# Kernel tuning notes

Hardware: AMD Instinct MI355X
Metric: run time of the kernel (lower is better)

Reference implementation:

```python
import jax, jax.numpy as jnp
import numpy as np

B, N, M = 262144, 8, 4  # batch, state dim, measurement dim


def _tril_square(x, n):
    """x: (b, n(n+1)/2) linearized lower-tri elems -> L @ L.T, (b, n, n)."""
    i, j = np.tril_indices(n)
    L = jnp.zeros((x.shape[0], n, n), dtype=x.dtype).at[:, i, j].set(x)
    return jnp.einsum('bik,bjk->bij', L, L)


def setup_inputs() -> dict:
    key = jax.random.key(0)
    ks = jax.random.split(key, 7)
    measurement = jax.random.normal(ks[0], (B, M), dtype=jnp.float32)
    state = jax.random.normal(ks[1], (B, N), dtype=jnp.float32)
    # SPD state covariance: A A^T / n + I
    A = jax.random.normal(ks[2], (B, N, N), dtype=jnp.float32) * 0.3
    state_cov = jnp.einsum('bik,bjk->bij', A, A) / N + jnp.eye(N, dtype=jnp.float32)
    F = jnp.eye(N, dtype=jnp.float32) + 0.1 * jax.random.normal(ks[3], (B, N, N), dtype=jnp.float32)
    H = jax.random.normal(ks[4], (B, M, N), dtype=jnp.float32) * 0.5
    process_noise = jax.random.normal(ks[5], (B, N * (N + 1) // 2), dtype=jnp.float32) * 0.1
    measurement_noise = jax.random.normal(ks[6], (B, M * (M + 1) // 2), dtype=jnp.float32) * 0.3
    return {
        'measurement': measurement, 'state': state, 'state_cov': state_cov,
        'F': F, 'H': H,
        'process_noise': process_noise, 'measurement_noise': measurement_noise,
    }


def reference(measurement, state, state_cov, F, H, process_noise, measurement_noise):
    b, n = state.shape
    m = measurement.shape[1]
    Q = _tril_square(process_noise, n)       # (b, n, n) process noise cov
    R = _tril_square(measurement_noise, m)   # (b, m, m) measurement noise cov

    # Predict
    new_state = jnp.einsum('bij,bj->bi', F, state)
    new_state_cov = jnp.einsum('bij,bjk,blk->bil', F, state_cov, F) + Q

    # Update
    prediction = jnp.einsum('bij,bj->bi', H, new_state)
    res = measurement - prediction
    res_cov = jnp.einsum('bij,bjk,blk->bil', H, new_state_cov, H) + R  # (b, m, m)
    PHt = jnp.einsum('bij,bkj->bik', new_state_cov, H)                 # (b, n, m)
    kgain = jnp.matmul(PHt, jnp.linalg.inv(res_cov))                   # (b, n, m)

    upd_state = new_state + jnp.einsum('bij,bj->bi', kgain, res)
    I = jnp.eye(n, dtype=state.dtype)
    upd_cov = jnp.matmul(I - jnp.matmul(kgain, H), new_state_cov)
    return prediction, upd_state, upd_cov
```

## Files before the change

### kernel.cpp

```cpp
#include <hip/hip_runtime.h>

#define DEVINL __device__ __forceinline__

#define TIX(i, j) ((i) * ((i) + 1) / 2 + (j))
#define SYM(arr, i, j) ((i) >= (j) ? arr[TIX(i, j)] : arr[TIX(j, i)])

DEVINL void inv4(const float* m, float* inv) {
    float s0 = m[0] * m[5] - m[1] * m[4];
    float s1 = m[0] * m[6] - m[2] * m[4];
    float s2 = m[0] * m[7] - m[3] * m[4];
    float s3 = m[1] * m[6] - m[2] * m[5];
    float s4 = m[1] * m[7] - m[3] * m[5];
    float s5 = m[2] * m[7] - m[3] * m[6];
    float c5 = m[10] * m[15] - m[11] * m[14];
    float c4 = m[9] * m[15] - m[11] * m[13];
    float c3 = m[9] * m[14] - m[10] * m[13];
    float c2 = m[8] * m[15] - m[11] * m[12];
    float c1 = m[8] * m[14] - m[10] * m[12];
    float c0 = m[8] * m[13] - m[9] * m[12];
    float det = s0 * c5 - s1 * c4 + s2 * c3 + s3 * c2 - s4 * c1 + s5 * c0;
    float id = 1.0f / det;
    inv[0]  = ( m[5] * c5 - m[6] * c4 + m[7] * c3) * id;
    inv[1]  = (-m[1] * c5 + m[2] * c4 - m[3] * c3) * id;
    inv[2]  = ( m[13] * s5 - m[14] * s4 + m[15] * s3) * id;
    inv[3]  = (-m[9] * s5 + m[10] * s4 - m[11] * s3) * id;
    inv[4]  = (-m[4] * c5 + m[6] * c2 - m[7] * c1) * id;
    inv[5]  = ( m[0] * c5 - m[2] * c2 + m[3] * c1) * id;
    inv[6]  = (-m[12] * s5 + m[14] * s2 - m[15] * s1) * id;
    inv[7]  = ( m[8] * s5 - m[10] * s2 + m[11] * s1) * id;
    inv[8]  = ( m[4] * c4 - m[5] * c2 + m[7] * c0) * id;
    inv[9]  = (-m[0] * c4 + m[1] * c2 - m[3] * c0) * id;
    inv[10] = ( m[12] * s4 - m[13] * s2 + m[15] * s0) * id;
    inv[11] = (-m[8] * s4 + m[9] * s2 - m[11] * s0) * id;
    inv[12] = (-m[4] * c3 + m[5] * c1 - m[6] * c0) * id;
    inv[13] = ( m[0] * c3 - m[1] * c1 + m[2] * c0) * id;
    inv[14] = (-m[12] * s3 + m[13] * s1 - m[14] * s0) * id;
    inv[15] = ( m[8] * s3 - m[9] * s1 + m[10] * s0) * id;
}

__global__ __launch_bounds__(64) void ekf_kernel(
    const float* __restrict__ meas,
    const float* __restrict__ state,
    const float* __restrict__ Pin,
    const float* __restrict__ Fin,
    const float* __restrict__ Hin,
    const float* __restrict__ pnin,
    const float* __restrict__ mnin,
    float* __restrict__ out_pred,
    float* __restrict__ out_state,
    float* __restrict__ out_cov)
{
    const int t  = threadIdx.x;
    const int bb = blockIdx.x * 64;
    const int b  = bb + t;

    __shared__ float4 buf[576];

    {
        const float4* g = reinterpret_cast<const float4*>(pnin) + (size_t)bb * 9;
        #pragma unroll
        for (int i = 0; i < 9; ++i) buf[i * 64 + t] = g[i * 64 + t];
    }
    __syncthreads();
    float Pn[36];
    {
        float Lq[36];
        #pragma unroll
        for (int q = 0; q < 9; ++q) {
            float4 v = buf[t * 9 + q];
            Lq[4 * q] = v.x; Lq[4 * q + 1] = v.y; Lq[4 * q + 2] = v.z; Lq[4 * q + 3] = v.w;
        }
        #pragma unroll
        for (int i = 0; i < 8; ++i)
            #pragma unroll
            for (int j = 0; j <= i; ++j) {
                float acc = 0.f;
                #pragma unroll
                for (int k = 0; k <= j; ++k)
                    acc += Lq[TIX(i, k)] * Lq[TIX(j, k)];
                Pn[TIX(i, j)] = acc;
            }
    }

    {
        const float4* g = reinterpret_cast<const float4*>(state) + (size_t)bb * 2;
        #pragma unroll
        for (int i = 0; i < 2; ++i) {
            int f = i * 64 + t;
            buf[(f >> 1) * 3 + (f & 1)] = g[f];
        }
    }
    __syncthreads();
    float s[8];
    {
        float4 a = buf[t * 3 + 0], c = buf[t * 3 + 1];
        s[0] = a.x; s[1] = a.y; s[2] = a.z; s[3] = a.w;
        s[4] = c.x; s[5] = c.y; s[6] = c.z; s[7] = c.w;
    }

    float Ps[36];
    #pragma unroll
    for (int h = 0; h < 2; ++h) {
        {
            const float4* g = reinterpret_cast<const float4*>(Pin) + (size_t)bb * 16;
            #pragma unroll
            for (int i = 0; i < 8; ++i) {
                int fl = i * 64 + t;
                int bq = fl >> 3, q = fl & 7;
                buf[bq * 9 + q] = g[bq * 16 + 8 * h + q];
            }
        }
        __syncthreads();
        #pragma unroll
        for (int q = 0; q < 8; ++q) {
            float4 v = buf[t * 9 + q];
            const int row = 4 * h + (q >> 1), c0 = 4 * (q & 1);
            if (c0 + 0 <= row) Ps[TIX(row, c0 + 0)] = v.x;
            if (c0 + 1 <= row) Ps[TIX(row, c0 + 1)] = v.y;
            if (c0 + 2 <= row) Ps[TIX(row, c0 + 2)] = v.z;
            if (c0 + 3 <= row) Ps[TIX(row, c0 + 3)] = v.w;
        }
        __syncthreads();
    }

    float Fm[64];
    #pragma unroll
    for (int h = 0; h < 2; ++h) {
        {
            const float4* g = reinterpret_cast<const float4*>(Fin) + (size_t)bb * 16;
            #pragma unroll
            for (int i = 0; i < 8; ++i) {
                int fl = i * 64 + t;
                int bq = fl >> 3, q = fl & 7;
                buf[bq * 9 + q] = g[bq * 16 + 8 * h + q];
            }
        }
        __syncthreads();
        #pragma unroll
        for (int q = 0; q < 8; ++q) {
            float4 v = buf[t * 9 + q];
            Fm[32 * h + 4 * q + 0] = v.x;
            Fm[32 * h + 4 * q + 1] = v.y;
            Fm[32 * h + 4 * q + 2] = v.z;
            Fm[32 * h + 4 * q + 3] = v.w;
        }
        __syncthreads();
    }

    float ns[8];
    #pragma unroll
    for (int i = 0; i < 8; ++i) {
        float acc = 0.f;
        #pragma unroll
        for (int j = 0; j < 8; ++j) acc += Fm[i * 8 + j] * s[j];
        ns[i] = acc;
    }
    #pragma unroll
    for (int l = 0; l < 8; ++l) {
        float gcol[8];
        #pragma unroll
        for (int j = 0; j < 8; ++j) {
            float acc = 0.f;
            #pragma unroll
            for (int k = 0; k < 8; ++k) acc += SYM(Ps, j, k) * Fm[l * 8 + k];
            gcol[j] = acc;
        }
        #pragma unroll
        for (int i = l; i < 8; ++i) {
            float acc = Pn[TIX(i, l)];
            #pragma unroll
            for (int j = 0; j < 8; ++j) acc += Fm[i * 8 + j] * gcol[j];
            Pn[TIX(i, l)] = acc;
        }
    }

    float Hm[32];
    {
        const float4* g = reinterpret_cast<const float4*>(Hin) + (size_t)bb * 8;
        #pragma unroll
        for (int i = 0; i < 8; ++i) {
            int fl = i * 64 + t;
            buf[(fl >> 3) * 9 + (fl & 7)] = g[fl];
        }
    }
    __syncthreads();
    #pragma unroll
    for (int q = 0; q < 8; ++q) {
        float4 v = buf[t * 9 + q];
        Hm[4 * q + 0] = v.x; Hm[4 * q + 1] = v.y;
        Hm[4 * q + 2] = v.z; Hm[4 * q + 3] = v.w;
    }

    float res[4];
    {
        float4 z = *(reinterpret_cast<const float4*>(meas) + b);
        float pr[4];
        #pragma unroll
        for (int i = 0; i < 4; ++i) {
            float acc = 0.f;
            #pragma unroll
            for (int j = 0; j < 8; ++j) acc += Hm[i * 8 + j] * ns[j];
            pr[i] = acc;
        }
        res[0] = z.x - pr[0]; res[1] = z.y - pr[1];
        res[2] = z.z - pr[2]; res[3] = z.w - pr[3];
        *(reinterpret_cast<float4*>(out_pred) + b) =
            make_float4(pr[0], pr[1], pr[2], pr[3]);
    }

    float HP[32];
    #pragma unroll
    for (int i = 0; i < 4; ++i)
        #pragma unroll
        for (int k = 0; k < 8; ++k) {
            float acc = 0.f;
            #pragma unroll
            for (int j = 0; j < 8; ++j) acc += Hm[i * 8 + j] * SYM(Pn, j, k);
            HP[i * 8 + k] = acc;
        }

    float Sf[16];
    #pragma unroll
    for (int i = 0; i < 4; ++i)
        #pragma unroll
        for (int l = 0; l <= i; ++l) {
            float acc = 0.f;
            #pragma unroll
            for (int k = 0; k < 8; ++k) acc += HP[i * 8 + k] * Hm[l * 8 + k];
            Sf[i * 4 + l] = acc;
            Sf[l * 4 + i] = acc;
        }

    {
        const float2* g = reinterpret_cast<const float2*>(mnin) + (size_t)bb * 5;
        float2* buf2 = reinterpret_cast<float2*>(buf);
        #pragma unroll
        for (int i = 0; i < 5; ++i) buf2[i * 64 + t] = g[i * 64 + t];
    }
    __syncthreads();
    float Si[16];
    {
        const float2* buf2 = reinterpret_cast<const float2*>(buf);
        float Lr[10];
        #pragma unroll
        for (int p = 0; p < 5; ++p) {
            float2 v = buf2[t * 5 + p];
            Lr[2 * p] = v.x; Lr[2 * p + 1] = v.y;
        }
        #pragma unroll
        for (int i = 0; i < 4; ++i)
            #pragma unroll
            for (int j = 0; j <= i; ++j) {
                float acc = 0.f;
                #pragma unroll
                for (int k = 0; k <= j; ++k)
                    acc += Lr[TIX(i, k)] * Lr[TIX(j, k)];
                Sf[i * 4 + j] += acc;
                if (i != j) Sf[j * 4 + i] += acc;
            }
        inv4(Sf, Si);
    }

    float us[8];
    {
        float w[4];
        #pragma unroll
        for (int a = 0; a < 4; ++a) {
            float acc = 0.f;
            #pragma unroll
            for (int c = 0; c < 4; ++c) acc += Si[a * 4 + c] * res[c];
            w[a] = acc;
        }
        #pragma unroll
        for (int i = 0; i < 8; ++i) {
            float acc = ns[i];
            #pragma unroll
            for (int a = 0; a < 4; ++a) acc += HP[a * 8 + i] * w[a];
            us[i] = acc;
        }
    }

    buf[t * 3 + 0] = make_float4(us[0], us[1], us[2], us[3]);
    buf[t * 3 + 1] = make_float4(us[4], us[5], us[6], us[7]);
    __syncthreads();
    {
        float4* g = reinterpret_cast<float4*>(out_state) + (size_t)bb * 2;
        #pragma unroll
        for (int i = 0; i < 2; ++i) {
            int f = i * 64 + t;
            g[f] = buf[(f >> 1) * 3 + (f & 1)];
        }
    }

    {
        float M[32];
        #pragma unroll
        for (int a = 0; a < 4; ++a)
            #pragma unroll
            for (int j = 0; j < 8; ++j) {
                float acc = 0.f;
                #pragma unroll
                for (int c = 0; c < 4; ++c) acc += Si[a * 4 + c] * HP[c * 8 + j];
                M[a * 8 + j] = acc;
            }
        #pragma unroll
        for (int i = 0; i < 8; ++i)
            #pragma unroll
            for (int l = 0; l <= i; ++l) {
                float acc = Pn[TIX(i, l)];
                #pragma unroll
                for (int a = 0; a < 4; ++a) acc -= HP[a * 8 + i] * M[a * 8 + l];
                Pn[TIX(i, l)] = acc;
            }
    }

    #pragma unroll
    for (int h = 0; h < 2; ++h) {
        #pragma unroll
        for (int r = 0; r < 4; ++r) {
            const int i = 4 * h + r;
            buf[t * 9 + 2 * r + 0] = make_float4(SYM(Pn, i, 0), SYM(Pn, i, 1),
                                                 SYM(Pn, i, 2), SYM(Pn, i, 3));
            buf[t * 9 + 2 * r + 1] = make_float4(SYM(Pn, i, 4), SYM(Pn, i, 5),
                                                 SYM(Pn, i, 6), SYM(Pn, i, 7));
        }
        __syncthreads();
        {
            float4* g = reinterpret_cast<float4*>(out_cov) + (size_t)bb * 16;
            #pragma unroll
            for (int i = 0; i < 8; ++i) {
                int fl = i * 64 + t;
                int bq = fl >> 3, q = fl & 7;
                g[bq * 16 + 8 * h + q] = buf[bq * 9 + q];
            }
        }
        __syncthreads();
    }
}

extern "C" void kernel_launch(void* const* d_in, const int* in_sizes, int n_in,
                              void* d_out, int out_size, void* d_ws, size_t ws_size,
                              hipStream_t stream) {
    const float* meas  = (const float*)d_in[0];
    const float* state = (const float*)d_in[1];
    const float* Pin   = (const float*)d_in[2];
    const float* Fin   = (const float*)d_in[3];
    const float* Hin   = (const float*)d_in[4];
    const float* pn    = (const float*)d_in[5];
    const float* mn    = (const float*)d_in[6];

    const int B = in_sizes[1] / 8;

    float* out = (float*)d_out;
    float* out_pred  = out;
    float* out_state = out + (size_t)B * 4;
    float* out_cov   = out + (size_t)B * 12;

    dim3 block(64);
    dim3 grid(B / 64);
    ekf_kernel<<<grid, block, 0, stream>>>(meas, state, Pin, Fin, Hin, pn, mn,
                                           out_pred, out_state, out_cov);
}
```

Baseline: 256.0 us.

## Issue all input loads up front via global_load_lds with XOR swizzle and vmcnt waits

All per-batch input matrices (process noise, P, F, H) are now loaded asynchronously straight into LDS with global_load_lds at kernel start, each into its own LDS region. A staged s_waitcnt vmcnt lets compute on earlier inputs overlap with later loads, replacing the earlier sequence of load, barrier, read. An XOR swizzle on the 16-byte chunks avoids LDS bank conflicts, and the state, measurement and measurement noise vectors are now read directly per thread. The cost is a much larger LDS footprint (about 50KB per 64-thread block), which may reduce occupancy, plus reliance on exact vmcnt counting, which is fragile.

```diff
diff --git a/kernel.cpp b/kernel.cpp
--- a/kernel.cpp
+++ b/kernel.cpp
@@ -4,6 +4,14 @@
 
 #define TIX(i, j) ((i) * ((i) + 1) / 2 + (j))
 #define SYM(arr, i, j) ((i) >= (j) ? arr[TIX(i, j)] : arr[TIX(j, i)])
+
+#define MEMFENCE() asm volatile("" ::: "memory")
+#define VMCNT(n) asm volatile("s_waitcnt vmcnt(" #n ")" ::: "memory")
+
+#define GLOAD16(gsrc, ldst)                                        \
+    __builtin_amdgcn_global_load_lds(                              \
+        (const __attribute__((address_space(1))) void*)(gsrc),     \
+        (__attribute__((address_space(3))) void*)(ldst), 16, 0, 0)
 
 DEVINL void inv4(const float* m, float* inv) {
     float s0 = m[0] * m[5] - m[1] * m[4];
@@ -53,21 +61,64 @@
     const int t  = threadIdx.x;
     const int bb = blockIdx.x * 64;
     const int b  = bb + t;
-
-    __shared__ float4 buf[576];
+    const int tx = t & 7;
+
+    __shared__ float4 arena[3136];
+    float4* pn4 = arena;
+    float4* P4  = arena + 576;
+    float4* F4  = arena + 1600;
+    float4* H4  = arena + 2624;
+    float4* st4 = arena + 576;
+    float4* cv4 = arena + 1600;
+
+    float s[8];
+    {
+        const float4* g = reinterpret_cast<const float4*>(state) + (size_t)b * 2;
+        float4 a = g[0], c = g[1];
+        s[0] = a.x; s[1] = a.y; s[2] = a.z; s[3] = a.w;
+        s[4] = c.x; s[5] = c.y; s[6] = c.z; s[7] = c.w;
+    }
+    MEMFENCE();
 
     {
         const float4* g = reinterpret_cast<const float4*>(pnin) + (size_t)bb * 9;
         #pragma unroll
-        for (int i = 0; i < 9; ++i) buf[i * 64 + t] = g[i * 64 + t];
-    }
-    __syncthreads();
+        for (int i = 0; i < 9; ++i)
+            GLOAD16(g + (i * 64 + t), pn4 + i * 64);
+    }
+    {
+        const float4* g = reinterpret_cast<const float4*>(Pin) + (size_t)bb * 16;
+        #pragma unroll
+        for (int i = 0; i < 16; ++i) {
+            int f = i * 64 + t, bq = f >> 4, qp = f & 15;
+            GLOAD16(g + ((bq << 4) | (qp ^ (bq & 7))), P4 + i * 64);
+        }
+    }
+    {
+        const float4* g = reinterpret_cast<const float4*>(Fin) + (size_t)bb * 16;
+        #pragma unroll
+        for (int i = 0; i < 16; ++i) {
+            int f = i * 64 + t, bq = f >> 4, qp = f & 15;
+            GLOAD16(g + ((bq << 4) | (qp ^ (bq & 7))), F4 + i * 64);
+        }
+    }
+    {
+        const float4* g = reinterpret_cast<const float4*>(Hin) + (size_t)bb * 8;
+        #pragma unroll
+        for (int i = 0; i < 8; ++i) {
+            int f = i * 64 + t, bq = f >> 3, qp = f & 7;
+            GLOAD16(g + ((bq << 3) | (qp ^ (bq & 7))), H4 + i * 64);
+        }
+    }
+    MEMFENCE();
+
+    VMCNT(38);
     float Pn[36];
     {
         float Lq[36];
         #pragma unroll
         for (int q = 0; q < 9; ++q) {
-            float4 v = buf[t * 9 + q];
+            float4 v = pn4[t * 9 + q];
             Lq[4 * q] = v.x; Lq[4 * q + 1] = v.y; Lq[4 * q + 2] = v.z; Lq[4 * q + 3] = v.w;
         }
         #pragma unroll
@@ -82,70 +133,39 @@
             }
     }
 
-    {
-        const float4* g = reinterpret_cast<const float4*>(state) + (size_t)bb * 2;
-        #pragma unroll
-        for (int i = 0; i < 2; ++i) {
-            int f = i * 64 + t;
-            buf[(f >> 1) * 3 + (f & 1)] = g[f];
-        }
-    }
-    __syncthreads();
-    float s[8];
-    {
-        float4 a = buf[t * 3 + 0], c = buf[t * 3 + 1];
-        s[0] = a.x; s[1] = a.y; s[2] = a.z; s[3] = a.w;
-        s[4] = c.x; s[5] = c.y; s[6] = c.z; s[7] = c.w;
-    }
-
+    VMCNT(22);
     float Ps[36];
     #pragma unroll
-    for (int h = 0; h < 2; ++h) {
-        {
-            const float4* g = reinterpret_cast<const float4*>(Pin) + (size_t)bb * 16;
-            #pragma unroll
-            for (int i = 0; i < 8; ++i) {
-                int fl = i * 64 + t;
-                int bq = fl >> 3, q = fl & 7;
-                buf[bq * 9 + q] = g[bq * 16 + 8 * h + q];
-            }
-        }
-        __syncthreads();
-        #pragma unroll
-        for (int q = 0; q < 8; ++q) {
-            float4 v = buf[t * 9 + q];
-            const int row = 4 * h + (q >> 1), c0 = 4 * (q & 1);
-            if (c0 + 0 <= row) Ps[TIX(row, c0 + 0)] = v.x;
-            if (c0 + 1 <= row) Ps[TIX(row, c0 + 1)] = v.y;
-            if (c0 + 2 <= row) Ps[TIX(row, c0 + 2)] = v.z;
-            if (c0 + 3 <= row) Ps[TIX(row, c0 + 3)] = v.w;
-        }
-        __syncthreads();
-    }
-
+    for (int q = 0; q < 16; ++q) {
+        float4 v = P4[t * 16 + (q ^ tx)];
+        const int row = q >> 1, c0 = (q & 1) * 4;
+        if (c0 + 0 <= row) Ps[TIX(row, c0 + 0)] = v.x;
+        if (c0 + 1 <= row) Ps[TIX(row, c0 + 1)] = v.y;
+        if (c0 + 2 <= row) Ps[TIX(row, c0 + 2)] = v.z;
+        if (c0 + 3 <= row) Ps[TIX(row, c0 + 3)] = v.w;
+    }
+
+    VMCNT(6);
     float Fm[64];
     #pragma unroll
-    for (int h = 0; h < 2; ++h) {
-        {
-            const float4* g = reinterpret_cast<const float4*>(Fin) + (size_t)bb * 16;
-            #pragma unroll
-            for (int i = 0; i < 8; ++i) {
-                int fl = i * 64 + t;
-                int bq = fl >> 3, q = fl & 7;
-                buf[bq * 9 + q] = g[bq * 16 + 8 * h + q];
-            }
-        }
-        __syncthreads();
-        #pragma unroll
-        for (int q = 0; q < 8; ++q) {
-            float4 v = buf[t * 9 + q];
-            Fm[32 * h + 4 * q + 0] = v.x;
-            Fm[32 * h + 4 * q + 1] = v.y;
-            Fm[32 * h + 4 * q + 2] = v.z;
-            Fm[32 * h + 4 * q + 3] = v.w;
-        }
-        __syncthreads();
-    }
+    for (int q = 0; q < 16; ++q) {
+        float4 v = F4[t * 16 + (q ^ tx)];
+        Fm[4 * q + 0] = v.x; Fm[4 * q + 1] = v.y;
+        Fm[4 * q + 2] = v.z; Fm[4 * q + 3] = v.w;
+    }
+
+    MEMFENCE();
+    float4 z = *(reinterpret_cast<const float4*>(meas) + b);
+    float Lr[10];
+    {
+        const float2* g = reinterpret_cast<const float2*>(mnin) + (size_t)b * 5;
+        #pragma unroll
+        for (int p = 0; p < 5; ++p) {
+            float2 v = g[p];
+            Lr[2 * p] = v.x; Lr[2 * p + 1] = v.y;
+        }
+    }
+    MEMFENCE();
 
     float ns[8];
     #pragma unroll
@@ -174,26 +194,17 @@
         }
     }
 
+    VMCNT(0);
     float Hm[32];
-    {
-        const float4* g = reinterpret_cast<const float4*>(Hin) + (size_t)bb * 8;
-        #pragma unroll
-        for (int i = 0; i < 8; ++i) {
-            int fl = i * 64 + t;
-            buf[(fl >> 3) * 9 + (fl & 7)] = g[fl];
-        }
-    }
-    __syncthreads();
     #pragma unroll
     for (int q = 0; q < 8; ++q) {
-        float4 v = buf[t * 9 + q];
+        float4 v = H4[t * 8 + (q ^ tx)];
         Hm[4 * q + 0] = v.x; Hm[4 * q + 1] = v.y;
         Hm[4 * q + 2] = v.z; Hm[4 * q + 3] = v.w;
     }
 
     float res[4];
     {
-        float4 z = *(reinterpret_cast<const float4*>(meas) + b);
         float pr[4];
         #pragma unroll
         for (int i = 0; i < 4; ++i) {
@@ -219,34 +230,19 @@
             HP[i * 8 + k] = acc;
         }
 
-    float Sf[16];
-    #pragma unroll
-    for (int i = 0; i < 4; ++i)
-        #pragma unroll
-        for (int l = 0; l <= i; ++l) {
-            float acc = 0.f;
-            #pragma unroll
-            for (int k = 0; k < 8; ++k) acc += HP[i * 8 + k] * Hm[l * 8 + k];
-            Sf[i * 4 + l] = acc;
-            Sf[l * 4 + i] = acc;
-        }
-
-    {
-        const float2* g = reinterpret_cast<const float2*>(mnin) + (size_t)bb * 5;
-        float2* buf2 = reinterpret_cast<float2*>(buf);
-        #pragma unroll
-        for (int i = 0; i < 5; ++i) buf2[i * 64 + t] = g[i * 64 + t];
-    }
-    __syncthreads();
     float Si[16];
     {
-        const float2* buf2 = reinterpret_cast<const float2*>(buf);
-        float Lr[10];
-        #pragma unroll
-        for (int p = 0; p < 5; ++p) {
-            float2 v = buf2[t * 5 + p];
-            Lr[2 * p] = v.x; Lr[2 * p + 1] = v.y;
-        }
+        float Sf[16];
+        #pragma unroll
+        for (int i = 0; i < 4; ++i)
+            #pragma unroll
+            for (int l = 0; l <= i; ++l) {
+                float acc = 0.f;
+                #pragma unroll
+                for (int k = 0; k < 8; ++k) acc += HP[i * 8 + k] * Hm[l * 8 + k];
+                Sf[i * 4 + l] = acc;
+                Sf[l * 4 + i] = acc;
+            }
         #pragma unroll
         for (int i = 0; i < 4; ++i)
             #pragma unroll
@@ -280,15 +276,15 @@
         }
     }
 
-    buf[t * 3 + 0] = make_float4(us[0], us[1], us[2], us[3]);
-    buf[t * 3 + 1] = make_float4(us[4], us[5], us[6], us[7]);
+    st4[t * 3 + 0] = make_float4(us[0], us[1], us[2], us[3]);
+    st4[t * 3 + 1] = make_float4(us[4], us[5], us[6], us[7]);
     __syncthreads();
     {
         float4* g = reinterpret_cast<float4*>(out_state) + (size_t)bb * 2;
         #pragma unroll
         for (int i = 0; i < 2; ++i) {
             int f = i * 64 + t;
-            g[f] = buf[(f >> 1) * 3 + (f & 1)];
+            g[f] = st4[(f >> 1) * 3 + (f & 1)];
         }
     }
 
@@ -316,12 +312,13 @@
 
     #pragma unroll
     for (int h = 0; h < 2; ++h) {
+        __syncthreads();
         #pragma unroll
         for (int r = 0; r < 4; ++r) {
             const int i = 4 * h + r;
-            buf[t * 9 + 2 * r + 0] = make_float4(SYM(Pn, i, 0), SYM(Pn, i, 1),
+            cv4[t * 9 + 2 * r + 0] = make_float4(SYM(Pn, i, 0), SYM(Pn, i, 1),
                                                  SYM(Pn, i, 2), SYM(Pn, i, 3));
-            buf[t * 9 + 2 * r + 1] = make_float4(SYM(Pn, i, 4), SYM(Pn, i, 5),
+            cv4[t * 9 + 2 * r + 1] = make_float4(SYM(Pn, i, 4), SYM(Pn, i, 5),
                                                  SYM(Pn, i, 6), SYM(Pn, i, 7));
         }
         __syncthreads();
@@ -331,10 +328,9 @@
             for (int i = 0; i < 8; ++i) {
                 int fl = i * 64 + t;
                 int bq = fl >> 3, q = fl & 7;
-                g[bq * 16 + 8 * h + q] = buf[bq * 9 + q];
-            }
-        }
-        __syncthreads();
+                g[bq * 16 + 8 * h + q] = cv4[bq * 9 + q];
+            }
+        }
     }
 }
 
```

New measurement: 259.0 us. Within noise of the previous version (+1.2%).

## Split each batch element across two lanes to halve per-thread register footprint

Applied to the files above, without the earlier changes.

Each Kalman filter instance is now processed by two threads (lanes q and q+32), each owning four columns of the covariance. Cross-half values (F rows, HP, the S partial sums, the predicted state) are exchanged with __shfl_xor. This cuts per-thread register use and raises occupancy via launch_bounds(64,4). Staging is reorganised so P and F each load in one pass, and Q, H and R share the shared-memory arena. The cost is redundant work in both halves (full Ps, inverse) plus extra shuffles, and the grid is doubled.

```diff
diff --git a/kernel.cpp b/kernel.cpp
--- a/kernel.cpp
+++ b/kernel.cpp
@@ -38,7 +38,7 @@
     inv[15] = ( m[8] * s3 - m[9] * s1 + m[10] * s0) * id;
 }
 
-__global__ __launch_bounds__(64) void ekf_kernel(
+__global__ __launch_bounds__(64, 4) void ekf_kernel(
     const float* __restrict__ meas,
     const float* __restrict__ state,
     const float* __restrict__ Pin,
@@ -51,201 +51,225 @@
     float* __restrict__ out_cov)
 {
     const int t  = threadIdx.x;
-    const int bb = blockIdx.x * 64;
-    const int b  = bb + t;
-
-    __shared__ float4 buf[576];
+    const int q  = t & 31;
+    const int p  = t >> 5;
+    const bool hi = (p != 0);
+    const int bb = blockIdx.x * 32;
+    const int b  = bb + q;
+
+    __shared__ float4 arena[576];
+
+    {
+        const float4* g = reinterpret_cast<const float4*>(state) + (size_t)bb * 2;
+        arena[(t >> 1) * 3 + (t & 1)] = g[t];
+    }
+    float4 z = *(reinterpret_cast<const float4*>(meas) + b);
+    __syncthreads();
+    float s_[8];
+    {
+        float4 a = arena[q * 3 + 0], c = arena[q * 3 + 1];
+        s_[0] = a.x; s_[1] = a.y; s_[2] = a.z; s_[3] = a.w;
+        s_[4] = c.x; s_[5] = c.y; s_[6] = c.z; s_[7] = c.w;
+    }
+
+    {
+        const float4* g = reinterpret_cast<const float4*>(Pin) + (size_t)bb * 16;
+        #pragma unroll
+        for (int i = 0; i < 8; ++i) {
+            int f = i * 64 + t;
+            arena[(f >> 4) * 17 + (f & 15)] = g[f];
+        }
+    }
+    __syncthreads();
+    float Ps[36];
+    #pragma unroll
+    for (int sI = 0; sI < 16; ++sI) {
+        float4 v = arena[q * 17 + sI];
+        const int row = sI >> 1, c0 = (sI & 1) * 4;
+        if (c0 + 0 <= row) Ps[TIX(row, c0 + 0)] = v.x;
+        if (c0 + 1 <= row) Ps[TIX(row, c0 + 1)] = v.y;
+        if (c0 + 2 <= row) Ps[TIX(row, c0 + 2)] = v.z;
+        if (c0 + 3 <= row) Ps[TIX(row, c0 + 3)] = v.w;
+    }
+
+    {
+        const float4* g = reinterpret_cast<const float4*>(Fin) + (size_t)bb * 16;
+        #pragma unroll
+        for (int i = 0; i < 8; ++i) {
+            int f = i * 64 + t;
+            arena[(f >> 4) * 17 + (f & 15)] = g[f];
+        }
+    }
+    __syncthreads();
+    float Fh[32];
+    #pragma unroll
+    for (int j = 0; j < 8; ++j) {
+        float4 v = arena[q * 17 + 8 * p + j];
+        const int r = j >> 1, c0 = 4 * (j & 1);
+        Fh[r * 8 + c0 + 0] = v.x; Fh[r * 8 + c0 + 1] = v.y;
+        Fh[r * 8 + c0 + 2] = v.z; Fh[r * 8 + c0 + 3] = v.w;
+    }
+
+    float ns_own[4];
+    #pragma unroll
+    for (int r = 0; r < 4; ++r) {
+        float acc = 0.f;
+        #pragma unroll
+        for (int k = 0; k < 8; ++k) acc += Fh[r * 8 + k] * s_[k];
+        ns_own[r] = acc;
+    }
+    float Gc[32];
+    #pragma unroll
+    for (int j = 0; j < 8; ++j)
+        #pragma unroll
+        for (int lr = 0; lr < 4; ++lr) {
+            float acc = 0.f;
+            #pragma unroll
+            for (int k = 0; k < 8; ++k) acc += SYM(Ps, j, k) * Fh[lr * 8 + k];
+            Gc[j * 4 + lr] = acc;
+        }
+
+    float Pnc[32];
+    #pragma unroll
+    for (int i = 0; i < 8; ++i) {
+        const int r = i & 3;
+        const bool own = ((i >> 2) == p);
+        float fr[8];
+        #pragma unroll
+        for (int k = 0; k < 8; ++k) {
+            float sh = __shfl_xor(Fh[r * 8 + k], 32);
+            fr[k] = own ? Fh[r * 8 + k] : sh;
+        }
+        #pragma unroll
+        for (int lr = 0; lr < 4; ++lr) {
+            float acc = 0.f;
+            #pragma unroll
+            for (int j = 0; j < 8; ++j) acc += fr[j] * Gc[j * 4 + lr];
+            Pnc[i * 4 + lr] = acc;
+        }
+    }
 
     {
         const float4* g = reinterpret_cast<const float4*>(pnin) + (size_t)bb * 9;
         #pragma unroll
-        for (int i = 0; i < 9; ++i) buf[i * 64 + t] = g[i * 64 + t];
-    }
-    __syncthreads();
-    float Pn[36];
+        for (int i = 0; i < 5; ++i) {
+            int f = i * 64 + t;
+            if (f < 288) arena[f] = g[f];
+        }
+        const float4* gh = reinterpret_cast<const float4*>(Hin) + (size_t)bb * 8;
+        #pragma unroll
+        for (int i = 0; i < 4; ++i) {
+            int f = i * 64 + t;
+            arena[288 + (f >> 3) * 9 + (f & 7)] = gh[f];
+        }
+    }
+    __syncthreads();
+
     {
         float Lq[36];
         #pragma unroll
-        for (int q = 0; q < 9; ++q) {
-            float4 v = buf[t * 9 + q];
-            Lq[4 * q] = v.x; Lq[4 * q + 1] = v.y; Lq[4 * q + 2] = v.z; Lq[4 * q + 3] = v.w;
-        }
+        for (int rr = 0; rr < 9; ++rr) {
+            float4 v = arena[q * 9 + rr];
+            Lq[4 * rr + 0] = v.x; Lq[4 * rr + 1] = v.y;
+            Lq[4 * rr + 2] = v.z; Lq[4 * rr + 3] = v.w;
+        }
+        float Ld[32];
+        #pragma unroll
+        for (int lr = 0; lr < 4; ++lr)
+            #pragma unroll
+            for (int k = 0; k < 8; ++k) {
+                float lo  = (k <= lr)     ? Lq[TIX(lr, k)]     : 0.f;
+                float hif = (k <= 4 + lr) ? Lq[TIX(4 + lr, k)] : 0.f;
+                Ld[lr * 8 + k] = hi ? hif : lo;
+            }
         #pragma unroll
         for (int i = 0; i < 8; ++i)
             #pragma unroll
-            for (int j = 0; j <= i; ++j) {
-                float acc = 0.f;
+            for (int lr = 0; lr < 4; ++lr) {
+                float acc = Pnc[i * 4 + lr];
                 #pragma unroll
-                for (int k = 0; k <= j; ++k)
-                    acc += Lq[TIX(i, k)] * Lq[TIX(j, k)];
-                Pn[TIX(i, j)] = acc;
+                for (int k = 0; k < 8; ++k) {
+                    if (k <= i && k <= 4 + lr)
+                        acc += Lq[TIX(i, k)] * Ld[lr * 8 + k];
+                }
+                Pnc[i * 4 + lr] = acc;
             }
     }
 
-    {
-        const float4* g = reinterpret_cast<const float4*>(state) + (size_t)bb * 2;
-        #pragma unroll
-        for (int i = 0; i < 2; ++i) {
-            int f = i * 64 + t;
-            buf[(f >> 1) * 3 + (f & 1)] = g[f];
-        }
-    }
-    __syncthreads();
-    float s[8];
-    {
-        float4 a = buf[t * 3 + 0], c = buf[t * 3 + 1];
-        s[0] = a.x; s[1] = a.y; s[2] = a.z; s[3] = a.w;
-        s[4] = c.x; s[5] = c.y; s[6] = c.z; s[7] = c.w;
-    }
-
-    float Ps[36];
-    #pragma unroll
-    for (int h = 0; h < 2; ++h) {
-        {
-            const float4* g = reinterpret_cast<const float4*>(Pin) + (size_t)bb * 16;
-            #pragma unroll
-            for (int i = 0; i < 8; ++i) {
-                int fl = i * 64 + t;
-                int bq = fl >> 3, q = fl & 7;
-                buf[bq * 9 + q] = g[bq * 16 + 8 * h + q];
-            }
-        }
-        __syncthreads();
-        #pragma unroll
-        for (int q = 0; q < 8; ++q) {
-            float4 v = buf[t * 9 + q];
-            const int row = 4 * h + (q >> 1), c0 = 4 * (q & 1);
-            if (c0 + 0 <= row) Ps[TIX(row, c0 + 0)] = v.x;
-            if (c0 + 1 <= row) Ps[TIX(row, c0 + 1)] = v.y;
-            if (c0 + 2 <= row) Ps[TIX(row, c0 + 2)] = v.z;
-            if (c0 + 3 <= row) Ps[TIX(row, c0 + 3)] = v.w;
-        }
-        __syncthreads();
-    }
-
-    float Fm[64];
-    #pragma unroll
-    for (int h = 0; h < 2; ++h) {
-        {
-            const float4* g = reinterpret_cast<const float4*>(Fin) + (size_t)bb * 16;
-            #pragma unroll
-            for (int i = 0; i < 8; ++i) {
-                int fl = i * 64 + t;
-                int bq = fl >> 3, q = fl & 7;
-                buf[bq * 9 + q] = g[bq * 16 + 8 * h + q];
-            }
-        }
-        __syncthreads();
-        #pragma unroll
-        for (int q = 0; q < 8; ++q) {
-            float4 v = buf[t * 9 + q];
-            Fm[32 * h + 4 * q + 0] = v.x;
-            Fm[32 * h + 4 * q + 1] = v.y;
-            Fm[32 * h + 4 * q + 2] = v.z;
-            Fm[32 * h + 4 * q + 3] = v.w;
-        }
-        __syncthreads();
-    }
-
-    float ns[8];
-    #pragma unroll
-    for (int i = 0; i < 8; ++i) {
+    float Hm[32];
+    #pragma unroll
+    for (int j = 0; j < 8; ++j) {
+        float4 v = arena[288 + q * 9 + j];
+        const int r = j >> 1, c0 = 4 * (j & 1);
+        Hm[r * 8 + c0 + 0] = v.x; Hm[r * 8 + c0 + 1] = v.y;
+        Hm[r * 8 + c0 + 2] = v.z; Hm[r * 8 + c0 + 3] = v.w;
+    }
+
+    float nsf[8];
+    #pragma unroll
+    for (int r = 0; r < 4; ++r) {
+        float sh = __shfl_xor(ns_own[r], 32);
+        nsf[r]     = hi ? sh : ns_own[r];
+        nsf[4 + r] = hi ? ns_own[r] : sh;
+    }
+
+    float res[4], pr[4];
+    #pragma unroll
+    for (int i = 0; i < 4; ++i) {
         float acc = 0.f;
         #pragma unroll
-        for (int j = 0; j < 8; ++j) acc += Fm[i * 8 + j] * s[j];
-        ns[i] = acc;
-    }
-    #pragma unroll
-    for (int l = 0; l < 8; ++l) {
-        float gcol[8];
-        #pragma unroll
-        for (int j = 0; j < 8; ++j) {
-            float acc = 0.f;
-            #pragma unroll
-            for (int k = 0; k < 8; ++k) acc += SYM(Ps, j, k) * Fm[l * 8 + k];
-            gcol[j] = acc;
-        }
-        #pragma unroll
-        for (int i = l; i < 8; ++i) {
-            float acc = Pn[TIX(i, l)];
-            #pragma unroll
-            for (int j = 0; j < 8; ++j) acc += Fm[i * 8 + j] * gcol[j];
-            Pn[TIX(i, l)] = acc;
-        }
-    }
-
-    float Hm[32];
-    {
-        const float4* g = reinterpret_cast<const float4*>(Hin) + (size_t)bb * 8;
-        #pragma unroll
-        for (int i = 0; i < 8; ++i) {
-            int fl = i * 64 + t;
-            buf[(fl >> 3) * 9 + (fl & 7)] = g[fl];
-        }
-    }
-    __syncthreads();
-    #pragma unroll
-    for (int q = 0; q < 8; ++q) {
-        float4 v = buf[t * 9 + q];
-        Hm[4 * q + 0] = v.x; Hm[4 * q + 1] = v.y;
-        Hm[4 * q + 2] = v.z; Hm[4 * q + 3] = v.w;
-    }
-
-    float res[4];
-    {
-        float4 z = *(reinterpret_cast<const float4*>(meas) + b);
-        float pr[4];
-        #pragma unroll
-        for (int i = 0; i < 4; ++i) {
-            float acc = 0.f;
-            #pragma unroll
-            for (int j = 0; j < 8; ++j) acc += Hm[i * 8 + j] * ns[j];
-            pr[i] = acc;
-        }
-        res[0] = z.x - pr[0]; res[1] = z.y - pr[1];
-        res[2] = z.z - pr[2]; res[3] = z.w - pr[3];
+        for (int j = 0; j < 8; ++j) acc += Hm[i * 8 + j] * nsf[j];
+        pr[i] = acc;
+    }
+    res[0] = z.x - pr[0]; res[1] = z.y - pr[1];
+    res[2] = z.z - pr[2]; res[3] = z.w - pr[3];
+    if (!hi)
         *(reinterpret_cast<float4*>(out_pred) + b) =
             make_float4(pr[0], pr[1], pr[2], pr[3]);
-    }
-
-    float HP[32];
-    #pragma unroll
-    for (int i = 0; i < 4; ++i)
-        #pragma unroll
-        for (int k = 0; k < 8; ++k) {
+
+    float HPc[16];
+    #pragma unroll
+    for (int a = 0; a < 4; ++a)
+        #pragma unroll
+        for (int lr = 0; lr < 4; ++lr) {
             float acc = 0.f;
             #pragma unroll
-            for (int j = 0; j < 8; ++j) acc += Hm[i * 8 + j] * SYM(Pn, j, k);
-            HP[i * 8 + k] = acc;
+            for (int j = 0; j < 8; ++j) acc += Hm[a * 8 + j] * Pnc[j * 4 + lr];
+            HPc[a * 4 + lr] = acc;
         }
 
     float Sf[16];
     #pragma unroll
-    for (int i = 0; i < 4; ++i)
-        #pragma unroll
-        for (int l = 0; l <= i; ++l) {
-            float acc = 0.f;
-            #pragma unroll
-            for (int k = 0; k < 8; ++k) acc += HP[i * 8 + k] * Hm[l * 8 + k];
-            Sf[i * 4 + l] = acc;
-            Sf[l * 4 + i] = acc;
-        }
-
-    {
+    for (int a = 0; a < 4; ++a)
+        #pragma unroll
+        for (int c = 0; c < 4; ++c) {
+            float part = 0.f;
+            #pragma unroll
+            for (int kl = 0; kl < 4; ++kl) {
+                float hv = hi ? Hm[c * 8 + 4 + kl] : Hm[c * 8 + kl];
+                part += HPc[a * 4 + kl] * hv;
+            }
+            Sf[a * 4 + c] = part + __shfl_xor(part, 32);
+        }
+
+    {
+        float2* a2 = reinterpret_cast<float2*>(arena);
         const float2* g = reinterpret_cast<const float2*>(mnin) + (size_t)bb * 5;
-        float2* buf2 = reinterpret_cast<float2*>(buf);
-        #pragma unroll
-        for (int i = 0; i < 5; ++i) buf2[i * 64 + t] = g[i * 64 + t];
+        #pragma unroll
+        for (int i = 0; i < 3; ++i) {
+            int f = i * 64 + t;
+            if (f < 160) a2[f] = g[f];
+        }
     }
     __syncthreads();
     float Si[16];
     {
-        const float2* buf2 = reinterpret_cast<const float2*>(buf);
+        const float2* a2 = reinterpret_cast<const float2*>(arena);
         float Lr[10];
         #pragma unroll
-        for (int p = 0; p < 5; ++p) {
-            float2 v = buf2[t * 5 + p];
-            Lr[2 * p] = v.x; Lr[2 * p + 1] = v.y;
+        for (int rr = 0; rr < 5; ++rr) {
+            float2 v = a2[q * 5 + rr];
+            Lr[2 * rr] = v.x; Lr[2 * rr + 1] = v.y;
         }
         #pragma unroll
         for (int i = 0; i < 4; ++i)
@@ -261,80 +285,68 @@
         inv4(Sf, Si);
     }
 
-    float us[8];
-    {
-        float w[4];
+    float w[4];
+    #pragma unroll
+    for (int a = 0; a < 4; ++a) {
+        float acc = 0.f;
+        #pragma unroll
+        for (int c = 0; c < 4; ++c) acc += Si[a * 4 + c] * res[c];
+        w[a] = acc;
+    }
+    float us[4];
+    #pragma unroll
+    for (int r = 0; r < 4; ++r) {
+        float acc = ns_own[r];
+        #pragma unroll
+        for (int a = 0; a < 4; ++a) acc += HPc[a * 4 + r] * w[a];
+        us[r] = acc;
+    }
+    arena[q * 3 + p] = make_float4(us[0], us[1], us[2], us[3]);
+    __syncthreads();
+    {
+        float4* g = reinterpret_cast<float4*>(out_state) + (size_t)bb * 2;
+        g[t] = arena[(t >> 1) * 3 + (t & 1)];
+    }
+
+    float M[16];
+    #pragma unroll
+    for (int a = 0; a < 4; ++a)
+        #pragma unroll
+        for (int lr = 0; lr < 4; ++lr) {
+            float acc = 0.f;
+            #pragma unroll
+            for (int c = 0; c < 4; ++c) acc += Si[a * 4 + c] * HPc[c * 4 + lr];
+            M[a * 4 + lr] = acc;
+        }
+    #pragma unroll
+    for (int i = 0; i < 8; ++i) {
+        const int r = i & 3;
+        const bool own = ((i >> 2) == p);
+        float hp[4];
         #pragma unroll
         for (int a = 0; a < 4; ++a) {
-            float acc = 0.f;
-            #pragma unroll
-            for (int c = 0; c < 4; ++c) acc += Si[a * 4 + c] * res[c];
-            w[a] = acc;
-        }
+            float sh = __shfl_xor(HPc[a * 4 + r], 32);
+            hp[a] = own ? HPc[a * 4 + r] : sh;
+        }
+        float cv[4];
+        #pragma unroll
+        for (int lr = 0; lr < 4; ++lr) {
+            float acc = Pnc[i * 4 + lr];
+            #pragma unroll
+            for (int a = 0; a < 4; ++a) acc -= hp[a] * M[a * 4 + lr];
+            cv[lr] = acc;
+        }
+        arena[q * 16 + ((i * 2 + p) ^ (q & 7))] = make_float4(cv[0], cv[1], cv[2], cv[3]);
+    }
+    __syncthreads();
+    {
+        float4* g = reinterpret_cast<float4*>(out_cov) + (size_t)bb * 16;
         #pragma unroll
         for (int i = 0; i < 8; ++i) {
-            float acc = ns[i];
-            #pragma unroll
-            for (int a = 0; a < 4; ++a) acc += HP[a * 8 + i] * w[a];
-            us[i] = acc;
-        }
-    }
-
-    buf[t * 3 + 0] = make_float4(us[0], us[1], us[2], us[3]);
-    buf[t * 3 + 1] = make_float4(us[4], us[5], us[6], us[7]);
-    __syncthreads();
-    {
-        float4* g = reinterpret_cast<float4*>(out_state) + (size_t)bb * 2;
-        #pragma unroll
-        for (int i = 0; i < 2; ++i) {
-            int f = i * 64 + t;
-            g[f] = buf[(f >> 1) * 3 + (f & 1)];
-        }
-    }
-
-    {
-        float M[32];
-        #pragma unroll
-        for (int a = 0; a < 4; ++a)
-            #pragma unroll
-            for (int j = 0; j < 8; ++j) {
-                float acc = 0.f;
-                #pragma unroll
-                for (int c = 0; c < 4; ++c) acc += Si[a * 4 + c] * HP[c * 8 + j];
-                M[a * 8 + j] = acc;
-            }
-        #pragma unroll
-        for (int i = 0; i < 8; ++i)
-            #pragma unroll
-            for (int l = 0; l <= i; ++l) {
-                float acc = Pn[TIX(i, l)];
-                #pragma unroll
-                for (int a = 0; a < 4; ++a) acc -= HP[a * 8 + i] * M[a * 8 + l];
-                Pn[TIX(i, l)] = acc;
-            }
-    }
-
-    #pragma unroll
-    for (int h = 0; h < 2; ++h) {
-        #pragma unroll
-        for (int r = 0; r < 4; ++r) {
-            const int i = 4 * h + r;
-            buf[t * 9 + 2 * r + 0] = make_float4(SYM(Pn, i, 0), SYM(Pn, i, 1),
-                                                 SYM(Pn, i, 2), SYM(Pn, i, 3));
-            buf[t * 9 + 2 * r + 1] = make_float4(SYM(Pn, i, 4), SYM(Pn, i, 5),
-                                                 SYM(Pn, i, 6), SYM(Pn, i, 7));
-        }
-        __syncthreads();
-        {
-            float4* g = reinterpret_cast<float4*>(out_cov) + (size_t)bb * 16;
-            #pragma unroll
-            for (int i = 0; i < 8; ++i) {
-                int fl = i * 64 + t;
-                int bq = fl >> 3, q = fl & 7;
-                g[bq * 16 + 8 * h + q] = buf[bq * 9 + q];
-            }
-        }
-        __syncthreads();
+            int f = i * 64 + t;
+            int qq = f >> 4, ss = f & 15;
+            g[f] = arena[qq * 16 + (ss ^ (qq & 7))];
+        }
     }
 }
 
@@ -357,7 +369,7 @@
     float* out_cov   = out + (size_t)B * 12;
 
     dim3 block(64);
-    dim3 grid(B / 64);
+    dim3 grid(B / 32);
     ekf_kernel<<<grid, block, 0, stream>>>(meas, state, Pin, Fin, Hin, pn, mn,
                                            out_pred, out_state, out_cov);
 }
```

Result: slower. 477.6 us (+86.6%).
